# Optimization experiments

Measured on AMD Instinct MI355X. Metric: run time of the kernel, lower is better.

The kernel has to match this reference:

```python
import jax, jax.numpy as jnp
import numpy as np

N = 100000   # nodes
E = 3200000  # edges
F = 128      # input features
H1 = 128     # first_gcn_dimensions
H2 = 64      # second_gcn_dimensions
D1 = 64      # first_dense_neurons
D2 = 8       # second_dense_neurons
L = 10       # number_of_labels


def setup_inputs() -> dict:
    key = jax.random.key(0)
    ks = jax.random.split(key, 8)
    edges = jax.random.randint(ks[0], (2, E), 0, N)
    features = jax.random.normal(ks[1], (N, F), dtype=jnp.float32)
    s = lambda k, shape: jax.random.normal(k, shape, dtype=jnp.float32) * 0.05
    return dict(
        edges=edges, features=features,
        W1=s(ks[2], (F, H1)), b1=jnp.zeros((H1,), jnp.float32),
        W2=s(ks[3], (H1, H2)), b2=jnp.zeros((H2,), jnp.float32),
        Wf1=s(ks[4], (H2, D1)), bf1=jnp.zeros((D1,), jnp.float32),
        Wf2=s(ks[5], (D1, D2)), bf2=jnp.zeros((D2,), jnp.float32),
        Wl=s(ks[6], (H2 * D2, L)), bl=jnp.zeros((L,), jnp.float32),
    )


def gcn_conv(x, W, b, src, dst, n):
    # PyG GCNConv: x' = D^{-1/2} (A + I) D^{-1/2} (x W) + b  (self-loops already in src/dst)
    h = x @ W                                            # [N, out]
    deg = jax.ops.segment_sum(jnp.ones(dst.shape[0], x.dtype), dst, num_segments=n)
    dinv = jnp.where(deg > 0, jax.lax.rsqrt(deg), 0.0)   # deg^{-1/2}, 0 for isolated
    norm = dinv[src] * dinv[dst]                         # [E+N]
    agg = jax.ops.segment_sum(h[src] * norm[:, None], dst, num_segments=n)
    return agg + b


def reference(edges, features, W1, b1, W2, b2, Wf1, bf1, Wf2, bf2, Wl, bl):
    n = features.shape[0]
    loop = jnp.arange(n)
    src = jnp.concatenate([edges[0], loop])
    dst = jnp.concatenate([edges[1], loop])

    h1 = jax.nn.relu(gcn_conv(features, W1, b1, src, dst, n))  # [N, H1]
    h2 = gcn_conv(h1, W2, b2, src, dst, n)                     # [N, H2]

    a1 = jnp.tanh(h2 @ Wf1 + bf1)                              # [N, D1]
    att = jax.nn.softmax(a1 @ Wf2 + bf2, axis=0)               # softmax over nodes, [N, D2]

    graph_embedding = (att.T @ h2).reshape(1, -1)              # [1, D2*H2]
    P = att.T @ att - jnp.eye(att.shape[1], dtype=att.dtype)   # [D2, D2]
    penalty = jnp.sum(jnp.sqrt(jnp.sum(P * P, axis=1)))

    predictions = jax.nn.log_softmax(graph_embedding @ Wl + bl, axis=1)  # [1, L]
    return graph_embedding, penalty, predictions
```

## Files before the change

### kernel.cpp

```cpp
#include <hip/hip_runtime.h>
#include <hip/hip_bf16.h>
#include <math.h>

#define NNODES 100000
#define NEDGES 3200000
#define NBUK ((NNODES + 127) >> 7)
#define NCHUNK 128
#define EPC (NEDGES / NCHUNK)

typedef float floatx2 __attribute__((ext_vector_type(2)));

__device__ __forceinline__ unsigned short f2bf(float x) {
    unsigned u = __float_as_uint(x);
    unsigned r = u + 0x7FFFu + ((u >> 16) & 1u);
    return (unsigned short)(r >> 16);
}
__device__ __forceinline__ void unpack8_bf16(uint4 v, float* f) {
    f[0] = __uint_as_float(v.x << 16); f[1] = __uint_as_float(v.x & 0xFFFF0000u);
    f[2] = __uint_as_float(v.y << 16); f[3] = __uint_as_float(v.y & 0xFFFF0000u);
    f[4] = __uint_as_float(v.z << 16); f[5] = __uint_as_float(v.z & 0xFFFF0000u);
    f[6] = __uint_as_float(v.w << 16); f[7] = __uint_as_float(v.w & 0xFFFF0000u);
}

__device__ __forceinline__ void acc8_fp8(uint2 v, floatx2* a) {
    a[0] += __builtin_amdgcn_cvt_pk_f32_fp8(v.x, false);
    a[1] += __builtin_amdgcn_cvt_pk_f32_fp8(v.x, true);
    a[2] += __builtin_amdgcn_cvt_pk_f32_fp8(v.y, false);
    a[3] += __builtin_amdgcn_cvt_pk_f32_fp8(v.y, true);
}
__device__ __forceinline__ void acc4_fp8(unsigned v, floatx2* a) {
    a[0] += __builtin_amdgcn_cvt_pk_f32_fp8(v, false);
    a[1] += __builtin_amdgcn_cvt_pk_f32_fp8(v, true);
}

__global__ __launch_bounds__(1024) void chunk_hist_kernel(const int* __restrict__ dst,
                                                          int* __restrict__ hist) {
    __shared__ int h[NBUK];
    int c = blockIdx.x, t = threadIdx.x;
    for (int i = t; i < NBUK; i += 1024) h[i] = 0;
    __syncthreads();
    int e0 = c * EPC, e1 = e0 + EPC;
    for (int e = e0 + t; e < e1; e += 1024)
        atomicAdd(&h[dst[e] >> 7], 1);
    __syncthreads();
    for (int i = t; i < NBUK; i += 1024)
        hist[c * NBUK + i] = h[i];
}

__global__ void col_scan_kernel(int* __restrict__ hist, int* __restrict__ btot) {
    int t = blockIdx.x * 256 + threadIdx.x;
    if (t >= NBUK) return;
    int run = 0;
    for (int c = 0; c < NCHUNK; c++) {
        int idx = c * NBUK + t;
        int v = hist[idx];
        hist[idx] = run;
        run += v;
    }
    btot[t] = run;
}

__global__ void bucket_scan_kernel(const int* __restrict__ btot, int* __restrict__ bstart,
                                   int* __restrict__ row_start, float* __restrict__ smalls) {
    __shared__ int s[1024];
    int t = threadIdx.x;
    if (t < 592) smalls[t] = 0.0f;
    int v = (t < NBUK) ? btot[t] : 0;
    s[t] = v;
    __syncthreads();
    for (int off = 1; off < 1024; off <<= 1) {
        int x = (t >= off) ? s[t - off] : 0;
        __syncthreads();
        s[t] += x;
        __syncthreads();
    }
    if (t < NBUK) bstart[t] = s[t] - v;
    if (t == 0) {
        bstart[NBUK] = NEDGES;
        row_start[NNODES] = NEDGES;
    }
}

__global__ __launch_bounds__(1024) void chunk_scatter_kernel(const int* __restrict__ src,
                                                             const int* __restrict__ dst,
                                                             const int* __restrict__ hist,
                                                             const int* __restrict__ bstart,
                                                             int* __restrict__ ebuk) {
    __shared__ int cur[NBUK];
    int c = blockIdx.x, t = threadIdx.x;
    for (int i = t; i < NBUK; i += 1024)
        cur[i] = bstart[i] + hist[c * NBUK + i];
    __syncthreads();
    int e0 = c * EPC, e1 = e0 + EPC;
    for (int e = e0 + t; e < e1; e += 1024) {
        int d = dst[e];
        int pos = atomicAdd(&cur[d >> 7], 1);
        ebuk[pos] = src[e] | ((d & 127) << 20);
    }
}

__global__ __launch_bounds__(256) void build_kernel(const int* __restrict__ ebuk,
                                                    const int* __restrict__ bstart,
                                                    int* __restrict__ row_start,
                                                    float* __restrict__ dinv,
                                                    int* __restrict__ csr) {
    __shared__ int cnt[128];
    __shared__ int cur[128];
    int b = blockIdx.x;
    int t = threadIdx.x;
    int s0 = bstart[b], s1 = bstart[b + 1];
    if (t < 128) cnt[t] = 0;
    __syncthreads();
    for (int i = s0 + t; i < s1; i += 256)
        atomicAdd(&cnt[(ebuk[i] >> 20) & 127], 1);
    __syncthreads();
    if (t == 0) {
        int run = s0;
        for (int i = 0; i < 128; i++) { cur[i] = run; run += cnt[i]; }
    }
    __syncthreads();
    int node = b * 128 + t;
    if (t < 128 && node < NNODES) {
        row_start[node] = cur[t];
        dinv[node] = rsqrtf((float)cnt[t] + 1.0f);
    }
    __syncthreads();
    for (int i = s0 + t; i < s1; i += 256) {
        int v = ebuk[i];
        int pos = atomicAdd(&cur[(v >> 20) & 127], 1);
        csr[pos] = v & 0xFFFFF;
    }
}

template <int KIN, int KOUT, int TR>
__global__ __launch_bounds__(256) void gemm_stage_kernel(const float* __restrict__ A,
                                                         const float* __restrict__ W,
                                                         const float* __restrict__ rowscale,
                                                         unsigned char* __restrict__ stage,
                                                         int nrows) {
    constexpr int COLG = KOUT / 4;
    constexpr int ROWG = 256 / COLG;
    constexpr int R    = TR / ROWG;
    constexpr int LDK  = KIN + 4;
    __shared__ float As[TR][LDK];
    int block_row = blockIdx.x * TR;
    int tid = threadIdx.x;

    constexpr int C4 = KIN / 4;
    for (int idx = tid; idx < TR * C4; idx += 256) {
        int r = idx / C4, c = idx % C4;
        float4 v = make_float4(0.f, 0.f, 0.f, 0.f);
        if (block_row + r < nrows)
            v = *(const float4*)(A + (size_t)(block_row + r) * KIN + c * 4);
        *(float4*)(&As[r][c * 4]) = v;
    }
    __syncthreads();

    int cg = tid % COLG, rg = tid / COLG;
    int j  = cg * 4;
    int r0 = rg * R;
    float4 acc[R];
#pragma unroll
    for (int r = 0; r < R; r++) acc[r] = make_float4(0.f, 0.f, 0.f, 0.f);

#pragma unroll 4
    for (int k = 0; k < KIN; k++) {
        float4 w = *(const float4*)(W + (size_t)k * KOUT + j);
#pragma unroll
        for (int r = 0; r < R; r++) {
            float a = As[r0 + r][k];
            acc[r].x += a * w.x; acc[r].y += a * w.y;
            acc[r].z += a * w.z; acc[r].w += a * w.w;
        }
    }
#pragma unroll
    for (int r = 0; r < R; r++) {
        int row = block_row + r0 + r;
        if (row < nrows) {
            float d = rowscale[row];
            int pk = __builtin_amdgcn_cvt_pk_fp8_f32(acc[r].x * d, acc[r].y * d, 0, false);
            pk = __builtin_amdgcn_cvt_pk_fp8_f32(acc[r].z * d, acc[r].w * d, pk, true);
            *(unsigned*)(stage + (size_t)row * KOUT + j) = (unsigned)pk;
        }
    }
}

template <int KIN, int KOUT, int TR>
__global__ __launch_bounds__(256) void gemm_stage_bf16_kernel(const unsigned short* __restrict__ A,
                                                              const float* __restrict__ W,
                                                              const float* __restrict__ rowscale,
                                                              unsigned char* __restrict__ stage,
                                                              int nrows) {
    constexpr int COLG = KOUT / 4;
    constexpr int ROWG = 256 / COLG;
    constexpr int R    = TR / ROWG;
    constexpr int LDK  = KIN + 4;
    __shared__ float As[TR][LDK];
    int block_row = blockIdx.x * TR;
    int tid = threadIdx.x;

    constexpr int C8 = KIN / 8;
    for (int idx = tid; idx < TR * C8; idx += 256) {
        int r = idx / C8, c = idx % C8;
        float f[8];
        uint4 v = make_uint4(0, 0, 0, 0);
        if (block_row + r < nrows)
            v = *(const uint4*)(A + (size_t)(block_row + r) * KIN + c * 8);
        unpack8_bf16(v, f);
#pragma unroll
        for (int i = 0; i < 8; i++) As[r][c * 8 + i] = f[i];
    }
    __syncthreads();

    int cg = tid % COLG, rg = tid / COLG;
    int j  = cg * 4;
    int r0 = rg * R;
    float4 acc[R];
#pragma unroll
    for (int r = 0; r < R; r++) acc[r] = make_float4(0.f, 0.f, 0.f, 0.f);

#pragma unroll 4
    for (int k = 0; k < KIN; k++) {
        float4 w = *(const float4*)(W + (size_t)k * KOUT + j);
#pragma unroll
        for (int r = 0; r < R; r++) {
            float a = As[r0 + r][k];
            acc[r].x += a * w.x; acc[r].y += a * w.y;
            acc[r].z += a * w.z; acc[r].w += a * w.w;
        }
    }
#pragma unroll
    for (int r = 0; r < R; r++) {
        int row = block_row + r0 + r;
        if (row < nrows) {
            float d = rowscale[row];
            int pk = __builtin_amdgcn_cvt_pk_fp8_f32(acc[r].x * d, acc[r].y * d, 0, false);
            pk = __builtin_amdgcn_cvt_pk_fp8_f32(acc[r].z * d, acc[r].w * d, pk, true);
            *(unsigned*)(stage + (size_t)row * KOUT + j) = (unsigned)pk;
        }
    }
}

__global__ __launch_bounds__(256) void gather128_kernel(
    const unsigned char* __restrict__ hs, const int* __restrict__ row_start,
    const int* __restrict__ csr, const float* __restrict__ dinv,
    const float* __restrict__ bias, unsigned short* __restrict__ out) {
    int wave = threadIdx.x >> 6;
    int lane = threadIdx.x & 63;
    int n = blockIdx.x * 4 + wave;
    if (n >= NNODES) return;
    int g = lane >> 4;
    int c = lane & 15;
    unsigned cb = (unsigned)c << 3;
    int start = row_start[n], end = row_start[n + 1];
    floatx2 acc[4];
#pragma unroll
    for (int i = 0; i < 4; i++) acc[i] = (floatx2)(0.f);
    int w = (start + 3) & ~3;
    if (w > end) w = end;
    {
        int e2 = start + g;
        if (e2 < w) {
            unsigned o = ((unsigned)csr[e2] << 7) + cb;
            acc8_fp8(*(const uint2*)(hs + o), acc);
        }
    }
    for (; w + 16 <= end; w += 16) {
        int4 cs = *(const int4*)(csr + w + 4 * g);
        unsigned o0 = ((unsigned)cs.x << 7) + cb;
        unsigned o1 = ((unsigned)cs.y << 7) + cb;
        unsigned o2 = ((unsigned)cs.z << 7) + cb;
        unsigned o3 = ((unsigned)cs.w << 7) + cb;
        uint2 v0 = *(const uint2*)(hs + o0);
        uint2 v1 = *(const uint2*)(hs + o1);
        uint2 v2 = *(const uint2*)(hs + o2);
        uint2 v3 = *(const uint2*)(hs + o3);
        acc8_fp8(v0, acc);
        acc8_fp8(v1, acc);
        acc8_fp8(v2, acc);
        acc8_fp8(v3, acc);
    }
    for (int e2 = w + g; e2 < end; e2 += 4) {
        unsigned o = ((unsigned)csr[e2] << 7) + cb;
        acc8_fp8(*(const uint2*)(hs + o), acc);
    }
#pragma unroll
    for (int off = 16; off <= 32; off <<= 1)
#pragma unroll
        for (int i = 0; i < 4; i++) {
            acc[i].x += __shfl_xor(acc[i].x, off);
            acc[i].y += __shfl_xor(acc[i].y, off);
        }
    if (g == 0) {
        floatx2 s[4];
#pragma unroll
        for (int i = 0; i < 4; i++) s[i] = (floatx2)(0.f);
        acc8_fp8(*(const uint2*)(hs + (((unsigned)n << 7) + cb)), s);
        float d = dinv[n];
        int j = c * 8;
        float4 b0 = *(const float4*)(bias + j);
        float4 b1 = *(const float4*)(bias + j + 4);
        float r0 = fmaxf((acc[0].x + s[0].x) * d + b0.x, 0.f);
        float r1 = fmaxf((acc[0].y + s[0].y) * d + b0.y, 0.f);
        float r2 = fmaxf((acc[1].x + s[1].x) * d + b0.z, 0.f);
        float r3 = fmaxf((acc[1].y + s[1].y) * d + b0.w, 0.f);
        float r4 = fmaxf((acc[2].x + s[2].x) * d + b1.x, 0.f);
        float r5 = fmaxf((acc[2].y + s[2].y) * d + b1.y, 0.f);
        float r6 = fmaxf((acc[3].x + s[3].x) * d + b1.z, 0.f);
        float r7 = fmaxf((acc[3].y + s[3].y) * d + b1.w, 0.f);
        uint4 p;
        p.x = (unsigned)f2bf(r0) | ((unsigned)f2bf(r1) << 16);
        p.y = (unsigned)f2bf(r2) | ((unsigned)f2bf(r3) << 16);
        p.z = (unsigned)f2bf(r4) | ((unsigned)f2bf(r5) << 16);
        p.w = (unsigned)f2bf(r6) | ((unsigned)f2bf(r7) << 16);
        *(uint4*)(out + (((size_t)n << 7) + j)) = p;
    }
}

__global__ __launch_bounds__(256) void gather64_kernel(
    const unsigned char* __restrict__ hs, const int* __restrict__ row_start,
    const int* __restrict__ csr, const float* __restrict__ dinv,
    const float* __restrict__ bias, float* __restrict__ out) {
    int wave = threadIdx.x >> 6;
    int lane = threadIdx.x & 63;
    int n = blockIdx.x * 4 + wave;
    if (n >= NNODES) return;
    int g = lane >> 4;
    int c = lane & 15;
    unsigned cb = (unsigned)c << 2;
    int start = row_start[n], end = row_start[n + 1];
    floatx2 acc[2];
    acc[0] = (floatx2)(0.f); acc[1] = (floatx2)(0.f);
    int w = (start + 3) & ~3;
    if (w > end) w = end;
    {
        int e2 = start + g;
        if (e2 < w) {
            unsigned o = ((unsigned)csr[e2] << 6) + cb;
            acc4_fp8(*(const unsigned*)(hs + o), acc);
        }
    }
    for (; w + 16 <= end; w += 16) {
        int4 cs = *(const int4*)(csr + w + 4 * g);
        unsigned o0 = ((unsigned)cs.x << 6) + cb;
        unsigned o1 = ((unsigned)cs.y << 6) + cb;
        unsigned o2 = ((unsigned)cs.z << 6) + cb;
        unsigned o3 = ((unsigned)cs.w << 6) + cb;
        unsigned v0 = *(const unsigned*)(hs + o0);
        unsigned v1 = *(const unsigned*)(hs + o1);
        unsigned v2 = *(const unsigned*)(hs + o2);
        unsigned v3 = *(const unsigned*)(hs + o3);
        acc4_fp8(v0, acc);
        acc4_fp8(v1, acc);
        acc4_fp8(v2, acc);
        acc4_fp8(v3, acc);
    }
    for (int e2 = w + g; e2 < end; e2 += 4) {
        unsigned o = ((unsigned)csr[e2] << 6) + cb;
        acc4_fp8(*(const unsigned*)(hs + o), acc);
    }
#pragma unroll
    for (int off = 16; off <= 32; off <<= 1)
#pragma unroll
        for (int i = 0; i < 2; i++) {
            acc[i].x += __shfl_xor(acc[i].x, off);
            acc[i].y += __shfl_xor(acc[i].y, off);
        }
    if (g == 0) {
        floatx2 s[2];
        s[0] = (floatx2)(0.f); s[1] = (floatx2)(0.f);
        acc4_fp8(*(const unsigned*)(hs + (((unsigned)n << 6) + cb)), s);
        float d = dinv[n];
        int j = c * 4;
        float4 b4 = *(const float4*)(bias + j);
        float4 r;
        r.x = (acc[0].x + s[0].x) * d + b4.x;
        r.y = (acc[0].y + s[0].y) * d + b4.y;
        r.z = (acc[1].x + s[1].x) * d + b4.z;
        r.w = (acc[1].y + s[1].y) * d + b4.w;
        *(float4*)(out + (((size_t)n << 6) + j)) = r;
    }
}

__global__ __launch_bounds__(256) void attnpool_kernel(const float* __restrict__ h2,
                                                       const float* __restrict__ Wf1,
                                                       const float* __restrict__ bf1,
                                                       const float* __restrict__ Wf2,
                                                       const float* __restrict__ bf2,
                                                       float* __restrict__ ge,
                                                       float* __restrict__ ata,
                                                       float* __restrict__ colsum) {
    __shared__ float h2S[64][68];
    __shared__ float a1S[64][68];
    __shared__ float attS[64][8];
    __shared__ float colS[8][64];
    int t = threadIdx.x;
    int d0 = t >> 6;
    int j  = t & 63;
    int de = t >> 3, ee = t & 7;
    float accge0 = 0.f, accge1 = 0.f, accata = 0.f, acccol = 0.f;
    int ntiles = (NNODES + 63) / 64;
    for (int tile = blockIdx.x; tile < ntiles; tile += gridDim.x) {
        int base = tile * 64;
#pragma unroll
        for (int q = 0; q < 4; q++) {
            int idx = t + q * 256;
            int r = idx >> 4, cc = (idx & 15) * 4;
            int row = base + r;
            float4 v = (row < NNODES) ? *(const float4*)(h2 + (size_t)row * 64 + cc)
                                      : make_float4(0.f, 0.f, 0.f, 0.f);
            *(float4*)(&h2S[r][cc]) = v;
        }
        __syncthreads();
        {
            int cg = t & 15, rg = t >> 4;
            int jj = cg * 4, r0 = rg * 4;
            float4 b4 = *(const float4*)(bf1 + jj);
            float4 acc[4];
#pragma unroll
            for (int r = 0; r < 4; r++) acc[r] = b4;
#pragma unroll 4
            for (int k = 0; k < 64; k++) {
                float4 wv = *(const float4*)(Wf1 + (size_t)k * 64 + jj);
#pragma unroll
                for (int r = 0; r < 4; r++) {
                    float a = h2S[r0 + r][k];
                    acc[r].x += a * wv.x; acc[r].y += a * wv.y;
                    acc[r].z += a * wv.z; acc[r].w += a * wv.w;
                }
            }
#pragma unroll
            for (int r = 0; r < 4; r++) {
                a1S[r0 + r][jj]     = tanhf(acc[r].x);
                a1S[r0 + r][jj + 1] = tanhf(acc[r].y);
                a1S[r0 + r][jj + 2] = tanhf(acc[r].z);
                a1S[r0 + r][jj + 3] = tanhf(acc[r].w);
            }
        }
        __syncthreads();
        {
            int cc = t & 7, r = t >> 3;
#pragma unroll
            for (int h = 0; h < 2; h++) {
                int rr = r + h * 32;
                float acc = bf2[cc];
                for (int k = 0; k < 64; k++)
                    acc += a1S[rr][k] * Wf2[(size_t)k * 8 + cc];
                float ev = (base + rr < NNODES) ? __expf(acc) : 0.f;
                attS[rr][cc] = ev;
                colS[cc][rr] = ev;
            }
        }
        __syncthreads();
#pragma unroll 8
        for (int i = 0; i < 64; i++) {
            float hv = h2S[i][j];
            accge0 += attS[i][d0] * hv;
            accge1 += attS[i][d0 + 4] * hv;
        }
        if (t < 64) {
#pragma unroll 8
            for (int i = 0; i < 64; i++) accata += attS[i][de] * attS[i][ee];
        }
        if (t < 8) {
            float s = 0.f;
#pragma unroll
            for (int r = 0; r < 64; r++) s += colS[t][r];
            acccol += s;
        }
        __syncthreads();
    }
    atomicAdd(ge + d0 * 64 + j, accge0);
    atomicAdd(ge + (d0 + 4) * 64 + j, accge1);
    if (t < 64) atomicAdd(ata + de * 8 + ee, accata);
    if (t < 8) atomicAdd(colsum + t, acccol);
}

__global__ void final_kernel(const float* __restrict__ geacc, const float* __restrict__ ata,
                             const float* __restrict__ colsum, const float* __restrict__ Wl,
                             const float* __restrict__ bl, float* __restrict__ out) {
    __shared__ float geF[512];
    __shared__ float inv[8];
    __shared__ float logits[10];
    int t = threadIdx.x;
    if (t < 8) inv[t] = 1.0f / colsum[t];
    __syncthreads();
    for (int idx = t; idx < 512; idx += 64) {
        int d = idx >> 6;
        float v = geacc[idx] * inv[d];
        geF[idx] = v;
        out[idx] = v;
    }
    __syncthreads();
    if (t == 0) {
        float pen = 0.f;
        for (int d = 0; d < 8; d++) {
            float s = 0.f;
            for (int e = 0; e < 8; e++) {
                float p = ata[d * 8 + e] * inv[d] * inv[e] - (d == e ? 1.0f : 0.0f);
                s += p * p;
            }
            pen += sqrtf(s);
        }
        out[512] = pen;
    }
    if (t < 10) {
        float acc = bl[t];
        for (int k = 0; k < 512; k++) acc += geF[k] * Wl[(size_t)k * 10 + t];
        logits[t] = acc;
    }
    __syncthreads();
    if (t == 0) {
        float m = -INFINITY;
        for (int l = 0; l < 10; l++) m = fmaxf(m, logits[l]);
        float s = 0.f;
        for (int l = 0; l < 10; l++) s += expf(logits[l] - m);
        float ls = logf(s);
        for (int l = 0; l < 10; l++) out[513 + l] = logits[l] - m - ls;
    }
}

extern "C" void kernel_launch(void* const* d_in, const int* in_sizes, int n_in,
                              void* d_out, int out_size, void* d_ws, size_t ws_size,
                              hipStream_t stream) {
    const int* esrc = (const int*)d_in[0];
    const int* edst = esrc + NEDGES;
    const float* X   = (const float*)d_in[1];
    const float* W1  = (const float*)d_in[2];
    const float* b1  = (const float*)d_in[3];
    const float* W2  = (const float*)d_in[4];
    const float* b2  = (const float*)d_in[5];
    const float* Wf1 = (const float*)d_in[6];
    const float* bf1 = (const float*)d_in[7];
    const float* Wf2 = (const float*)d_in[8];
    const float* bf2 = (const float*)d_in[9];
    const float* Wl  = (const float*)d_in[10];
    const float* bl  = (const float*)d_in[11];
    float* out = (float*)d_out;

    float* ws     = (float*)d_ws;
    float* dinv   = ws;
    float* smalls = ws + 100352;
    float* colsum = smalls + 8;
    float* ata    = smalls + 16;
    float* geacc  = smalls + 80;
    float* A = ws + 101376;
    float* B = A + (size_t)NNODES * 128;
    int* row_start = (int*)(B + (size_t)NNODES * 128);
    int* btot      = row_start + 100352;
    int* bstart    = btot + 1024;
    int* csr       = bstart + 1024;
    int* ebuk      = (int*)A;
    int* hist      = (int*)B;
    unsigned char* stage = (unsigned char*)A;
    unsigned short* h1 = (unsigned short*)B;
    float* h2  = B;

    chunk_hist_kernel<<<NCHUNK, 1024, 0, stream>>>(edst, hist);
    col_scan_kernel<<<4, 256, 0, stream>>>(hist, btot);
    bucket_scan_kernel<<<1, 1024, 0, stream>>>(btot, bstart, row_start, smalls);
    chunk_scatter_kernel<<<NCHUNK, 1024, 0, stream>>>(esrc, edst, hist, bstart, ebuk);
    build_kernel<<<NBUK, 256, 0, stream>>>(ebuk, bstart, row_start, dinv, csr);

    gemm_stage_kernel<128, 128, 64><<<(NNODES + 63) / 64, 256, 0, stream>>>(X, W1, dinv, stage, NNODES);
    gather128_kernel<<<(NNODES + 3) / 4, 256, 0, stream>>>(stage, row_start, csr, dinv, b1, h1);

    gemm_stage_bf16_kernel<128, 64, 64><<<(NNODES + 63) / 64, 256, 0, stream>>>(h1, W2, dinv, stage, NNODES);
    gather64_kernel<<<(NNODES + 3) / 4, 256, 0, stream>>>(stage, row_start, csr, dinv, b2, h2);

    attnpool_kernel<<<512, 256, 0, stream>>>(h2, Wf1, bf1, Wf2, bf2, geacc, ata, colsum);
    final_kernel<<<1, 64, 0, stream>>>(geacc, ata, colsum, Wl, bl, out);
}
```

Measured before the change: 496.2 us.

## Parallelize CSR bucket scan, double edge chunks, unroll gathers by 32

The build kernel's serial single-thread prefix sum over 128 bucket counts is replaced by a parallel Hillis-Steele scan in shared memory. The number of edge chunks for the bucketing pass doubles, giving more blocks with fewer edges each. Both gather kernels gain a 32-edge unrolled loop that issues eight independent feature loads per lane, exposing more memory-level parallelism. The costs are extra barriers in the scan, a larger per-chunk histogram to build and scan, and higher register pressure in the gathers.

```diff
diff --git a/kernel.cpp b/kernel.cpp
--- a/kernel.cpp
+++ b/kernel.cpp
@@ -5,7 +5,7 @@
 #define NNODES 100000
 #define NEDGES 3200000
 #define NBUK ((NNODES + 127) >> 7)
-#define NCHUNK 128
+#define NCHUNK 256
 #define EPC (NEDGES / NCHUNK)
 
 typedef float floatx2 __attribute__((ext_vector_type(2)));
@@ -105,6 +105,7 @@
                                                     float* __restrict__ dinv,
                                                     int* __restrict__ csr) {
     __shared__ int cnt[128];
+    __shared__ int scn[128];
     __shared__ int cur[128];
     int b = blockIdx.x;
     int t = threadIdx.x;
@@ -114,15 +115,23 @@
     for (int i = s0 + t; i < s1; i += 256)
         atomicAdd(&cnt[(ebuk[i] >> 20) & 127], 1);
     __syncthreads();
-    if (t == 0) {
-        int run = s0;
-        for (int i = 0; i < 128; i++) { cur[i] = run; run += cnt[i]; }
-    }
-    __syncthreads();
+    if (t < 128) scn[t] = cnt[t];
+    __syncthreads();
+#pragma unroll
+    for (int off = 1; off < 128; off <<= 1) {
+        int x = (t < 128 && t >= off) ? scn[t - off] : 0;
+        __syncthreads();
+        if (t < 128) scn[t] += x;
+        __syncthreads();
+    }
     int node = b * 128 + t;
-    if (t < 128 && node < NNODES) {
-        row_start[node] = cur[t];
-        dinv[node] = rsqrtf((float)cnt[t] + 1.0f);
+    if (t < 128) {
+        int rs = s0 + scn[t] - cnt[t];
+        cur[t] = rs;
+        if (node < NNODES) {
+            row_start[node] = rs;
+            dinv[node] = rsqrtf((float)cnt[t] + 1.0f);
+        }
     }
     __syncthreads();
     for (int i = s0 + t; i < s1; i += 256) {
@@ -251,7 +260,7 @@
     if (n >= NNODES) return;
     int g = lane >> 4;
     int c = lane & 15;
-    unsigned cb = (unsigned)c << 3;
+    unsigned boff = (unsigned)c << 3;
     int start = row_start[n], end = row_start[n + 1];
     floatx2 acc[4];
 #pragma unroll
@@ -261,27 +270,34 @@
     {
         int e2 = start + g;
         if (e2 < w) {
-            unsigned o = ((unsigned)csr[e2] << 7) + cb;
+            unsigned o = ((unsigned)csr[e2] << 7) + boff;
             acc8_fp8(*(const uint2*)(hs + o), acc);
         }
+    }
+    for (; w + 32 <= end; w += 32) {
+        int4 ca = *(const int4*)(csr + w + 4 * g);
+        int4 cbv = *(const int4*)(csr + w + 16 + 4 * g);
+        uint2 v0 = *(const uint2*)(hs + (((unsigned)ca.x  << 7) + boff));
+        uint2 v1 = *(const uint2*)(hs + (((unsigned)ca.y  << 7) + boff));
+        uint2 v2 = *(const uint2*)(hs + (((unsigned)ca.z  << 7) + boff));
+        uint2 v3 = *(const uint2*)(hs + (((unsigned)ca.w  << 7) + boff));
+        uint2 v4 = *(const uint2*)(hs + (((unsigned)cbv.x << 7) + boff));
+        uint2 v5 = *(const uint2*)(hs + (((unsigned)cbv.y << 7) + boff));
+        uint2 v6 = *(const uint2*)(hs + (((unsigned)cbv.z << 7) + boff));
+        uint2 v7 = *(const uint2*)(hs + (((unsigned)cbv.w << 7) + boff));
+        acc8_fp8(v0, acc); acc8_fp8(v1, acc); acc8_fp8(v2, acc); acc8_fp8(v3, acc);
+        acc8_fp8(v4, acc); acc8_fp8(v5, acc); acc8_fp8(v6, acc); acc8_fp8(v7, acc);
     }
     for (; w + 16 <= end; w += 16) {
         int4 cs = *(const int4*)(csr + w + 4 * g);
-        unsigned o0 = ((unsigned)cs.x << 7) + cb;
-        unsigned o1 = ((unsigned)cs.y << 7) + cb;
-        unsigned o2 = ((unsigned)cs.z << 7) + cb;
-        unsigned o3 = ((unsigned)cs.w << 7) + cb;
-        uint2 v0 = *(const uint2*)(hs + o0);
-        uint2 v1 = *(const uint2*)(hs + o1);
-        uint2 v2 = *(const uint2*)(hs + o2);
-        uint2 v3 = *(const uint2*)(hs + o3);
-        acc8_fp8(v0, acc);
-        acc8_fp8(v1, acc);
-        acc8_fp8(v2, acc);
-        acc8_fp8(v3, acc);
+        uint2 v0 = *(const uint2*)(hs + (((unsigned)cs.x << 7) + boff));
+        uint2 v1 = *(const uint2*)(hs + (((unsigned)cs.y << 7) + boff));
+        uint2 v2 = *(const uint2*)(hs + (((unsigned)cs.z << 7) + boff));
+        uint2 v3 = *(const uint2*)(hs + (((unsigned)cs.w << 7) + boff));
+        acc8_fp8(v0, acc); acc8_fp8(v1, acc); acc8_fp8(v2, acc); acc8_fp8(v3, acc);
     }
     for (int e2 = w + g; e2 < end; e2 += 4) {
-        unsigned o = ((unsigned)csr[e2] << 7) + cb;
+        unsigned o = ((unsigned)csr[e2] << 7) + boff;
         acc8_fp8(*(const uint2*)(hs + o), acc);
     }
 #pragma unroll
@@ -295,7 +311,7 @@
         floatx2 s[4];
 #pragma unroll
         for (int i = 0; i < 4; i++) s[i] = (floatx2)(0.f);
-        acc8_fp8(*(const uint2*)(hs + (((unsigned)n << 7) + cb)), s);
+        acc8_fp8(*(const uint2*)(hs + (((unsigned)n << 7) + boff)), s);
         float d = dinv[n];
         int j = c * 8;
         float4 b0 = *(const float4*)(bias + j);
@@ -327,7 +343,7 @@
     if (n >= NNODES) return;
     int g = lane >> 4;
     int c = lane & 15;
-    unsigned cb = (unsigned)c << 2;
+    unsigned boff = (unsigned)c << 2;
     int start = row_start[n], end = row_start[n + 1];
     floatx2 acc[2];
     acc[0] = (floatx2)(0.f); acc[1] = (floatx2)(0.f);
@@ -336,27 +352,34 @@
     {
         int e2 = start + g;
         if (e2 < w) {
-            unsigned o = ((unsigned)csr[e2] << 6) + cb;
+            unsigned o = ((unsigned)csr[e2] << 6) + boff;
             acc4_fp8(*(const unsigned*)(hs + o), acc);
         }
+    }
+    for (; w + 32 <= end; w += 32) {
+        int4 ca = *(const int4*)(csr + w + 4 * g);
+        int4 cbv = *(const int4*)(csr + w + 16 + 4 * g);
+        unsigned v0 = *(const unsigned*)(hs + (((unsigned)ca.x  << 6) + boff));
+        unsigned v1 = *(const unsigned*)(hs + (((unsigned)ca.y  << 6) + boff));
+        unsigned v2 = *(const unsigned*)(hs + (((unsigned)ca.z  << 6) + boff));
+        unsigned v3 = *(const unsigned*)(hs + (((unsigned)ca.w  << 6) + boff));
+        unsigned v4 = *(const unsigned*)(hs + (((unsigned)cbv.x << 6) + boff));
+        unsigned v5 = *(const unsigned*)(hs + (((unsigned)cbv.y << 6) + boff));
+        unsigned v6 = *(const unsigned*)(hs + (((unsigned)cbv.z << 6) + boff));
+        unsigned v7 = *(const unsigned*)(hs + (((unsigned)cbv.w << 6) + boff));
+        acc4_fp8(v0, acc); acc4_fp8(v1, acc); acc4_fp8(v2, acc); acc4_fp8(v3, acc);
+        acc4_fp8(v4, acc); acc4_fp8(v5, acc); acc4_fp8(v6, acc); acc4_fp8(v7, acc);
     }
     for (; w + 16 <= end; w += 16) {
         int4 cs = *(const int4*)(csr + w + 4 * g);
-        unsigned o0 = ((unsigned)cs.x << 6) + cb;
-        unsigned o1 = ((unsigned)cs.y << 6) + cb;
-        unsigned o2 = ((unsigned)cs.z << 6) + cb;
-        unsigned o3 = ((unsigned)cs.w << 6) + cb;
-        unsigned v0 = *(const unsigned*)(hs + o0);
-        unsigned v1 = *(const unsigned*)(hs + o1);
-        unsigned v2 = *(const unsigned*)(hs + o2);
-        unsigned v3 = *(const unsigned*)(hs + o3);
-        acc4_fp8(v0, acc);
-        acc4_fp8(v1, acc);
-        acc4_fp8(v2, acc);
-        acc4_fp8(v3, acc);
+        unsigned v0 = *(const unsigned*)(hs + (((unsigned)cs.x << 6) + boff));
+        unsigned v1 = *(const unsigned*)(hs + (((unsigned)cs.y << 6) + boff));
+        unsigned v2 = *(const unsigned*)(hs + (((unsigned)cs.z << 6) + boff));
+        unsigned v3 = *(const unsigned*)(hs + (((unsigned)cs.w << 6) + boff));
+        acc4_fp8(v0, acc); acc4_fp8(v1, acc); acc4_fp8(v2, acc); acc4_fp8(v3, acc);
     }
     for (int e2 = w + g; e2 < end; e2 += 4) {
-        unsigned o = ((unsigned)csr[e2] << 6) + cb;
+        unsigned o = ((unsigned)csr[e2] << 6) + boff;
         acc4_fp8(*(const unsigned*)(hs + o), acc);
     }
 #pragma unroll
@@ -369,7 +392,7 @@
     if (g == 0) {
         floatx2 s[2];
         s[0] = (floatx2)(0.f); s[1] = (floatx2)(0.f);
-        acc4_fp8(*(const unsigned*)(hs + (((unsigned)n << 6) + cb)), s);
+        acc4_fp8(*(const unsigned*)(hs + (((unsigned)n << 6) + boff)), s);
         float d = dinv[n];
         int j = c * 4;
         float4 b4 = *(const float4*)(bias + j);
```

Measured after the change: 489.5 us. No clear change (-1.3%).
